# Performance work log

Measured on AMD Instinct MI355X. Metric: run time of the kernel, lower is better.

The kernel has to match this reference:

```python
import jax, jax.numpy as jnp
import numpy as np
import math

B, C, H, W = 16, 1, 1536, 1536


def setup_inputs() -> dict:
    key = jax.random.key(0)
    x = jax.random.normal(key, (B, C, H, W), dtype=jnp.float32)
    return {"inputs": x}


def _remove_nan(v):
    # utils.remove_nan: replace NaNs with zeros
    return jnp.where(jnp.isnan(v), jnp.zeros_like(v), v)


def reference(inputs):
    # Vectorized over batch; tf.map_fn applied axes 1,2 per-sample, which are
    # axes 2,3 (H, W) of the full (B, C, H, W) tensor.
    grad = lambda m, ax: jnp.roll(m, 1, axis=ax) - m
    p = grad(inputs, 2)          # d/dH
    q = grad(inputs, 3)          # d/dW
    r = grad(p, 2)               # d2/dH2
    s = grad(p, 3)               # d2/dHdW
    t = grad(q, 3)               # d2/dW2

    one_pq = 1.0 + p * p + q * q
    # mean curvature
    Hc = _remove_nan(-((1.0 + q * q) * r - 2.0 * p * q * s + (1.0 + p * p) * t)
                     / (2.0 * jnp.sqrt(one_pq ** 3)))
    # gaussian curvature
    Kc = _remove_nan((r * t - s * s) / (one_pq ** 2))

    root = jnp.sqrt(Hc * Hc - Kc)
    k_min = _remove_nan(Hc - root)
    k_max = _remove_nan(Hc + root)

    si = _remove_nan((2.0 / math.pi) * jnp.arctan((k_max + k_min) / (k_max - k_min)))
    return si
```

## Files before the change

kernel.cpp:

```cpp
#include <hip/hip_runtime.h>
#include <cmath>

#define B_ 16
#define H_ 1536
#define W_ 1536

__global__ __launch_bounds__(384) void ShapeIndex_kernel(
        const float* __restrict__ x, float* __restrict__ out) {
#pragma clang fp contract(off)
    const int h  = blockIdx.x;
    const int b  = blockIdx.y;
    const int w4 = threadIdx.x;
    const int w  = w4 * 4;

    const float* plane = x + (size_t)b * (H_ * W_);
    const int hm1 = (h == 0) ? (H_ - 1) : (h - 1);
    const int hm2 = (h <= 1) ? (h + H_ - 2) : (h - 2);

    const float4 vc = *(const float4*)(plane + h   * W_ + w);
    const float4 v1 = *(const float4*)(plane + hm1 * W_ + w);
    const float4 v2 = *(const float4*)(plane + hm2 * W_ + w);

    const int wm1 = (w == 0) ? (W_ - 1) : (w - 1);
    const int wm2 = (w == 0) ? (W_ - 2) : (w - 2);
    const float L0  = plane[h   * W_ + wm1];
    const float L1  = plane[h   * W_ + wm2];
    const float Lh1 = plane[hm1 * W_ + wm1];

    float c [4] = {vc.x, vc.y, vc.z, vc.w};
    float a1[4] = {v1.x, v1.y, v1.z, v1.w};
    float a2[4] = {v2.x, v2.y, v2.z, v2.w};
    float res[4];

#pragma unroll
    for (int j = 0; j < 4; ++j) {
        const float xc    = c[j];
        const float xh1   = a1[j];
        const float xh2   = a2[j];
        const float xw1   = (j > 0) ? c[j-1]  : L0;
        const float xw2   = (j > 1) ? c[j-2]  : ((j == 1) ? L0 : L1);
        const float xh1w1 = (j > 0) ? a1[j-1] : Lh1;

        const float p    = xh1   - xc;
        const float q    = xw1   - xc;
        const float p_up = xh2   - xh1;
        const float p_lf = xh1w1 - xw1;
        const float q_lf = xw2   - xw1;
        const float r = p_up - p;
        const float s = p_lf - p;
        const float t = q_lf - q;

        const float pp = p * p;
        const float qq = q * q;
        const float one_pq = (1.0f + pp) + qq;

        const float A = ((1.0f + qq) * r - ((2.0f * p) * q) * s)
                        + (1.0f + pp) * t;
        const float cube = (one_pq * one_pq) * one_pq;
        float Hc = -(A / (2.0f * sqrtf(cube)));
        if (Hc != Hc) Hc = 0.0f;

        const float sq = one_pq * one_pq;
        float Kc = (r * t - s * s) / sq;
        if (Kc != Kc) Kc = 0.0f;

        const float root = sqrtf(Hc * Hc - Kc);
        float kmin = Hc - root; if (kmin != kmin) kmin = 0.0f;
        float kmax = Hc + root; if (kmax != kmax) kmax = 0.0f;

        float si = 0.63661977236758134f * atanf((kmax + kmin) / (kmax - kmin));
        if (si != si) si = 0.0f;
        res[j] = si;
    }

    *(float4*)(out + (size_t)b * (H_ * W_) + h * W_ + w) =
        make_float4(res[0], res[1], res[2], res[3]);
}

extern "C" void kernel_launch(void* const* d_in, const int* in_sizes, int n_in,
                              void* d_out, int out_size, void* d_ws, size_t ws_size,
                              hipStream_t stream) {
    const float* x = (const float*)d_in[0];
    float* out = (float*)d_out;
    dim3 grid(H_, B_);
    dim3 block(384);
    ShapeIndex_kernel<<<grid, block, 0, stream>>>(x, out);
}
```

Measured before the change: 296.9 us.

## Vectorize shape-index math and replace atanf with polynomial approximation

Recasts the per-element computation with 4-wide ext_vector types so the compiler can emit packed float ops. It replaces the library atanf with a degree-11 minimax polynomial plus range reduction, and replaces the IEEE divide with a hardware reciprocal. The intermediate NaN scrubs on Hc, Kc, kmin and kmax are removed, keeping only a final NaN check. This lowers ALU cost in a kernel that may be partly compute-bound, at the cost of lower accuracy and NaN/inf semantics that can differ from the reference.

```diff
diff --git a/kernel.cpp b/kernel.cpp
--- a/kernel.cpp
+++ b/kernel.cpp
@@ -5,13 +5,14 @@
 #define H_ 1536
 #define W_ 1536
 
+typedef float v4f __attribute__((ext_vector_type(4)));
+
 __global__ __launch_bounds__(384) void ShapeIndex_kernel(
         const float* __restrict__ x, float* __restrict__ out) {
 #pragma clang fp contract(off)
     const int h  = blockIdx.x;
     const int b  = blockIdx.y;
-    const int w4 = threadIdx.x;
-    const int w  = w4 * 4;
+    const int w  = threadIdx.x * 4;
 
     const float* plane = x + (size_t)b * (H_ * W_);
     const int hm1 = (h == 0) ? (H_ - 1) : (h - 1);
@@ -27,51 +28,81 @@
     const float L1  = plane[h   * W_ + wm2];
     const float Lh1 = plane[hm1 * W_ + wm1];
 
-    float c [4] = {vc.x, vc.y, vc.z, vc.w};
-    float a1[4] = {v1.x, v1.y, v1.z, v1.w};
-    float a2[4] = {v2.x, v2.y, v2.z, v2.w};
-    float res[4];
+    const v4f xc    = {vc.x, vc.y, vc.z, vc.w};
+    const v4f xh1   = {v1.x, v1.y, v1.z, v1.w};
+    const v4f xh2   = {v2.x, v2.y, v2.z, v2.w};
+    const v4f xw1   = {L0,  vc.x, vc.y, vc.z};
+    const v4f xw2   = {L1,  L0,  vc.x, vc.y};
+    const v4f xh1w1 = {Lh1, v1.x, v1.y, v1.z};
 
+    const v4f p    = xh1   - xc;
+    const v4f q    = xw1   - xc;
+    const v4f p_up = xh2   - xh1;
+    const v4f p_lf = xh1w1 - xw1;
+    const v4f q_lf = xw2   - xw1;
+    const v4f r = p_up - p;
+    const v4f s = p_lf - p;
+    const v4f t = q_lf - q;
+
+    const v4f pp = p * p;
+    const v4f qq = q * q;
+    const v4f one_pq = (1.0f + pp) + qq;
+    const v4f A = ((1.0f + qq) * r - ((2.0f * p) * q) * s) + (1.0f + pp) * t;
+    const v4f sq   = one_pq * one_pq;
+    const v4f cube = sq * one_pq;
+    const v4f numk = r * t - s * s;
+
+    v4f Hc, Kc;
 #pragma unroll
     for (int j = 0; j < 4; ++j) {
-        const float xc    = c[j];
-        const float xh1   = a1[j];
-        const float xh2   = a2[j];
-        const float xw1   = (j > 0) ? c[j-1]  : L0;
-        const float xw2   = (j > 1) ? c[j-2]  : ((j == 1) ? L0 : L1);
-        const float xh1w1 = (j > 0) ? a1[j-1] : Lh1;
+        Hc[j] = -(A[j] / (2.0f * __builtin_sqrtf(cube[j])));
+        Kc[j] = numk[j] / sq[j];
+    }
 
-        const float p    = xh1   - xc;
-        const float q    = xw1   - xc;
-        const float p_up = xh2   - xh1;
-        const float p_lf = xh1w1 - xw1;
-        const float q_lf = xw2   - xw1;
-        const float r = p_up - p;
-        const float s = p_lf - p;
-        const float t = q_lf - q;
+    const v4f disc = Hc * Hc - Kc;
+    v4f root;
+#pragma unroll
+    for (int j = 0; j < 4; ++j) root[j] = __builtin_sqrtf(disc[j]);
 
-        const float pp = p * p;
-        const float qq = q * q;
-        const float one_pq = (1.0f + pp) + qq;
+    const v4f kmin = Hc - root;
+    const v4f kmax = Hc + root;
+    const v4f num  = kmax + kmin;
+    const v4f den  = kmax - kmin;
 
-        const float A = ((1.0f + qq) * r - ((2.0f * p) * q) * s)
-                        + (1.0f + pp) * t;
-        const float cube = (one_pq * one_pq) * one_pq;
-        float Hc = -(A / (2.0f * sqrtf(cube)));
-        if (Hc != Hc) Hc = 0.0f;
+    v4f z;
+#pragma unroll
+    for (int j = 0; j < 4; ++j) z[j] = num[j] * __builtin_amdgcn_rcpf(den[j]);
 
-        const float sq = one_pq * one_pq;
-        float Kc = (r * t - s * s) / sq;
-        if (Kc != Kc) Kc = 0.0f;
+    v4f u;
+    bool big[4];
+#pragma unroll
+    for (int j = 0; j < 4; ++j) {
+        const float az  = __builtin_fabsf(z[j]);
+        const float inv = __builtin_amdgcn_rcpf(az);
+        big[j] = az > 1.0f;
+        u[j]   = big[j] ? inv : az;
+    }
+    const v4f x2 = u * u;
+    const v4f C5 = -0.01172120f, C4 = 0.05265332f, C3 = -0.11643287f,
+              C2 = 0.19354346f,  C1 = -0.33262347f, C0 = 0.99997726f;
+    v4f pl = __builtin_elementwise_fma(x2, C5, C4);
+    pl = __builtin_elementwise_fma(x2, pl, C3);
+    pl = __builtin_elementwise_fma(x2, pl, C2);
+    pl = __builtin_elementwise_fma(x2, pl, C1);
+    pl = __builtin_elementwise_fma(x2, pl, C0);
+    const v4f a    = u * pl;
+    const v4f asub = 1.57079632679489662f - a;
 
-        const float root = sqrtf(Hc * Hc - Kc);
-        float kmin = Hc - root; if (kmin != kmin) kmin = 0.0f;
-        float kmax = Hc + root; if (kmax != kmax) kmax = 0.0f;
+    v4f rs;
+#pragma unroll
+    for (int j = 0; j < 4; ++j)
+        rs[j] = __builtin_copysignf(big[j] ? asub[j] : a[j], z[j]);
+    const v4f siv = 0.63661977236758134f * rs;
 
-        float si = 0.63661977236758134f * atanf((kmax + kmin) / (kmax - kmin));
-        if (si != si) si = 0.0f;
-        res[j] = si;
-    }
+    float res[4];
+#pragma unroll
+    for (int j = 0; j < 4; ++j)
+        res[j] = (siv[j] == siv[j]) ? siv[j] : 0.0f;
 
     *(float4*)(out + (size_t)b * (H_ * W_) + h * W_ + w) =
         make_float4(res[0], res[1], res[2], res[3]);
```

Measured after the change: 276.8 us. 6.8% less time.
